# Optimization experiments

Measured on AMD Instinct MI355X. Metric: run time of the kernel, lower is better.

## Reference

```python
import jax, jax.numpy as jnp
import numpy as np

D_MODEL = 1024
NUM_HEADS = 16
D_K = D_MODEL // NUM_HEADS
SCALE = float(np.sqrt(D_K))


def setup_inputs() -> dict:
    key = jax.random.key(0)
    ks = jax.random.split(key, 11)
    B, S, D = 2, 2048, D_MODEL
    def lin(kw):
        # xavier-uniform-ish weight, zero bias (matches torch init style)
        lim = float(np.sqrt(6.0 / (D + D)))
        return jax.random.uniform(kw, (D, D), jnp.float32, -lim, lim)
    return {
        "q": jax.random.normal(ks[0], (B, S, D), jnp.float32),
        "k": jax.random.normal(ks[1], (B, S, D), jnp.float32),
        "v": jax.random.normal(ks[2], (B, S, D), jnp.float32),
        "Wq": lin(ks[3]), "bq": jnp.zeros((D,), jnp.float32),
        "Wk": lin(ks[4]), "bk": jnp.zeros((D,), jnp.float32),
        "Wv": lin(ks[5]), "bv": jnp.zeros((D,), jnp.float32),
        "Wo": lin(ks[6]), "bo": jnp.zeros((D,), jnp.float32),
    }


def _split_heads(x):
    B, S, _ = x.shape
    return x.reshape(B, S, NUM_HEADS, D_K).transpose(0, 2, 1, 3)  # (B,H,S,dk)


def reference(q, k, v, Wq, bq, Wk, bk, Wv, bv, Wo, bo):
    # torch nn.Linear: y = x @ W.T + b
    Q = _split_heads(q @ Wq.T + bq)
    K = _split_heads(k @ Wk.T + bk)
    V = _split_heads(v @ Wv.T + bv)
    scores = jnp.einsum("bhqd,bhkd->bhqk", Q, K) / SCALE
    # numerically-stable softmax with detached max (as in the torch code)
    m = jax.lax.stop_gradient(jnp.max(scores, axis=-1, keepdims=True))
    exp_scores = jnp.exp(scores - m)
    attn = exp_scores / (jnp.sum(exp_scores, axis=-1, keepdims=True) + 1e-9)
    out = jnp.einsum("bhqk,bhkd->bhqd", attn, V)  # (B,H,S,dk)
    B, H, S, dk = out.shape
    out = out.transpose(0, 2, 1, 3).reshape(B, S, H * dk)
    return out @ Wo.T + bo
```

## Files before the change

### kernel.cpp

```cpp
#include <hip/hip_runtime.h>


#define D_MODEL 1024
#define NHEADS  16
#define DKH     64
#define SEQ     2048
#define BATCH   2
#define MTOT    (BATCH * SEQ)
#define XE      ((long)MTOT * D_MODEL)
#define WE      ((long)D_MODEL * D_MODEL)
#define QSCALE  0.18033688011112042f

typedef __attribute__((ext_vector_type(8))) short short8v;
typedef __attribute__((ext_vector_type(4))) short short4v;
typedef __attribute__((ext_vector_type(4))) float f32x4;

typedef __attribute__((address_space(1))) void as1_void;
typedef __attribute__((address_space(3))) void as3_void;

__device__ __forceinline__ void gload16(const void* g, void* l) {
    __builtin_amdgcn_global_load_lds((const as1_void*)g, (as3_void*)l, 16, 0, 0);
}

__device__ __forceinline__ unsigned short f2bf(float x) {
    unsigned int u = __float_as_uint(x);
    u += 0x7FFFu + ((u >> 16) & 1u);
    return (unsigned short)(u >> 16);
}

__device__ __forceinline__ float fexp2(float x) {
    return __builtin_amdgcn_exp2f(x);
}

__device__ __forceinline__ unsigned int cvt_pk_bf16(float lo, float hi) {
    unsigned int r;
    asm("v_cvt_pk_bf16_f32 %0, %1, %2" : "=v"(r) : "v"(lo), "v"(hi));
    return r;
}

__device__ __forceinline__ int swz_u(int row, int col) {
    int byte = (col << 1) ^ ((row & 7) << 4);
    return (row << 6) + (byte >> 1);
}

__device__ __forceinline__ int swz_v(int d, int kv) {
    int slot = (d & 6) | ((d >> 3) & 1);
    int byte = (kv << 1) ^ (slot << 4);
    return (d << 6) + (byte >> 1);
}

struct ConvArgs {
    const float*    src[4];
    unsigned short* dst[4];
    int             n4[4];
};

__global__ __launch_bounds__(256) void convert_kernel(ConvArgs a) {
    int z = blockIdx.y;
    const float4*   s = (const float4*)a.src[z];
    unsigned short* d = a.dst[z];
    int n = a.n4[z];
    for (int i = blockIdx.x * blockDim.x + threadIdx.x; i < n;
         i += gridDim.x * blockDim.x) {
        float4 v = s[i];
        ushort4 o;
        o.x = f2bf(v.x); o.y = f2bf(v.y); o.z = f2bf(v.z); o.w = f2bf(v.w);
        *(ushort4*)(d + 4L * i) = o;
    }
}

__global__ __launch_bounds__(256) void proj_kernel(
    const float* __restrict__ xq, const float* __restrict__ xk,
    const float* __restrict__ xv, const unsigned short* __restrict__ wb,
    const float* __restrict__ bq, const float* __restrict__ bk,
    const float* __restrict__ bv, unsigned short* __restrict__ qkv) {
    __shared__ unsigned short As[3 * 128 * 32];
    __shared__ unsigned short Bs[3 * 128 * 32];

    const int t    = threadIdx.x;
    const int lane = t & 63;
    const int w    = t >> 6;
    const int wm   = w >> 1, wn = w & 1;
    const int l15  = lane & 15, g = lane >> 4;

    const int bid = blockIdx.x;
    const int xcd = bid & 7;
    const int k   = bid >> 3;
    const int ty  = (xcd << 2) | (k & 3);
    const int tx  = (k >> 2) & 7;
    const int z   = k >> 5;
    const float* bias = (z == 0) ? bq : (z == 1) ? bk : bv;
    const float scale = (z == 0) ? QSCALE : 1.0f;

    const float* Af = (z == 0) ? xq : (z == 1) ? xk : xv;
    const unsigned short* Bm = wb + (long)z * WE;
    unsigned short*       C  = qkv + (long)z * XE;
    const long m0 = (long)ty * 128;
    const long n0 = (long)tx * 128;
    const int  K  = D_MODEL;

    f32x4 acc[4][4] = {};

    const int idx0 = t, idx1 = t + 256;
    const int r0 = idx0 >> 2, c0 = (idx0 & 3) * 8;
    const int r1 = idx1 >> 2, c1 = (idx1 & 3) * 8;

    float4 a0_[2], a1_[2];

#define PLOAD_A(k0)                                                        \
    {                                                                      \
        const float* s0 = Af + (m0 + r0) * K + (k0) + c0;                  \
        const float* s1 = Af + (m0 + r1) * K + (k0) + c1;                  \
        a0_[0] = *(const float4*)(s0);                                     \
        a1_[0] = *(const float4*)(s0 + 4);                                 \
        a0_[1] = *(const float4*)(s1);                                     \
        a1_[1] = *(const float4*)(s1 + 4);                                 \
    }

#define PSTAGE_B(k0, buf)                                                  \
    gload16(Bm + (n0 + r0) * K + (k0) + c0, &Bs[(buf) * 4096 + idx0 * 8]); \
    gload16(Bm + (n0 + r1) * K + (k0) + c1, &Bs[(buf) * 4096 + idx1 * 8]);

#define PWRITE_A(buf)                                                      \
    {                                                                      \
        uint4 pk;                                                          \
        pk.x = cvt_pk_bf16(a0_[0].x, a0_[0].y);                            \
        pk.y = cvt_pk_bf16(a0_[0].z, a0_[0].w);                            \
        pk.z = cvt_pk_bf16(a1_[0].x, a1_[0].y);                            \
        pk.w = cvt_pk_bf16(a1_[0].z, a1_[0].w);                            \
        *(uint4*)&As[(buf) * 4096 + idx0 * 8] = pk;                        \
        pk.x = cvt_pk_bf16(a0_[1].x, a0_[1].y);                            \
        pk.y = cvt_pk_bf16(a0_[1].z, a0_[1].w);                            \
        pk.z = cvt_pk_bf16(a1_[1].x, a1_[1].y);                            \
        pk.w = cvt_pk_bf16(a1_[1].z, a1_[1].w);                            \
        *(uint4*)&As[(buf) * 4096 + idx1 * 8] = pk;                        \
    }

    PLOAD_A(0);
    PSTAGE_B(0, 0);
    PWRITE_A(0);
    int cur = 0;

    for (int it = 0; it < K / 32; ++it) {
        const int nxt = (cur == 2) ? 0 : cur + 1;
        const int kn  = ((it + 1) * 32) & (K - 1);
        PLOAD_A(kn);
        PSTAGE_B(kn, nxt);
        asm volatile("s_waitcnt vmcnt(6)" ::: "memory");
        asm volatile("s_waitcnt lgkmcnt(0)" ::: "memory");
        __builtin_amdgcn_sched_barrier(0);
        __builtin_amdgcn_s_barrier();
        __builtin_amdgcn_sched_barrier(0);

        const unsigned short* Ab = &As[cur * 4096];
        const unsigned short* Bb = &Bs[cur * 4096];

        short8v af[4], bf_[4];
#pragma unroll
        for (int mf = 0; mf < 4; ++mf)
            af[mf] = *(const short8v*)&Ab[(wm * 64 + mf * 16 + l15) * 32 + g * 8];
#pragma unroll
        for (int nf = 0; nf < 4; ++nf)
            bf_[nf] = *(const short8v*)&Bb[(wn * 64 + nf * 16 + l15) * 32 + g * 8];
        __builtin_amdgcn_s_setprio(1);
#pragma unroll
        for (int mf = 0; mf < 4; ++mf)
#pragma unroll
            for (int nf = 0; nf < 4; ++nf)
                acc[mf][nf] = __builtin_amdgcn_mfma_f32_16x16x32_bf16(
                    af[mf], bf_[nf], acc[mf][nf], 0, 0, 0);
        __builtin_amdgcn_s_setprio(0);

        PWRITE_A(nxt);
        cur = nxt;
    }

    float bvv[4];
#pragma unroll
    for (int nf = 0; nf < 4; ++nf)
        bvv[nf] = bias[n0 + wn * 64 + nf * 16 + l15];

#pragma unroll
    for (int mf = 0; mf < 4; ++mf)
#pragma unroll
        for (int nf = 0; nf < 4; ++nf)
#pragma unroll
            for (int r = 0; r < 4; ++r) {
                long row = m0 + wm * 64 + mf * 16 + g * 4 + r;
                long col = n0 + wn * 64 + nf * 16 + l15;
                C[row * (long)D_MODEL + col] =
                    f2bf((acc[mf][nf][r] + bvv[nf]) * scale);
            }
#undef PLOAD_A
#undef PSTAGE_B
#undef PWRITE_A
}

__global__ __launch_bounds__(256) void out_kernel(
    const unsigned short* __restrict__ ob, const unsigned short* __restrict__ wo,
    const float* __restrict__ bo, float* __restrict__ out) {
    __shared__ unsigned short As[3 * 128 * 32];
    __shared__ unsigned short Bs[3 * 128 * 32];

    const int t    = threadIdx.x;
    const int lane = t & 63;
    const int w    = t >> 6;
    const int wm   = w >> 1, wn = w & 1;
    const int l15  = lane & 15, g = lane >> 4;

    const int bid = blockIdx.x;
    const int xcd = bid & 7;
    const int k   = bid >> 3;
    const long m0 = (long)((xcd << 2) | (k & 3)) * 128;
    const long n0 = (long)(k >> 2) * 128;
    const int  K  = D_MODEL, N = D_MODEL;

    f32x4 acc[4][4] = {};

    const int idx0 = t, idx1 = t + 256;
    const int r0 = idx0 >> 2, c0 = (idx0 & 3) * 8;
    const int r1 = idx1 >> 2, c1 = (idx1 & 3) * 8;
    const unsigned short* pa0 = ob + (m0 + r0) * K + c0;
    const unsigned short* pa1 = ob + (m0 + r1) * K + c1;
    const unsigned short* pb0 = wo + (n0 + r0) * K + c0;
    const unsigned short* pb1 = wo + (n0 + r1) * K + c1;

#define OSTAGE(k0, buf)                                                    \
    gload16(pa0 + (k0), &As[(buf) * 4096 + idx0 * 8]);                     \
    gload16(pa1 + (k0), &As[(buf) * 4096 + idx1 * 8]);                     \
    gload16(pb0 + (k0), &Bs[(buf) * 4096 + idx0 * 8]);                     \
    gload16(pb1 + (k0), &Bs[(buf) * 4096 + idx1 * 8]);

    OSTAGE(0, 0);
    int cur = 0;

    for (int it = 0; it < K / 32; ++it) {
        const int nxt = (cur == 2) ? 0 : cur + 1;
        const int kn  = ((it + 1) * 32) & (K - 1);
        OSTAGE(kn, nxt);
        asm volatile("s_waitcnt vmcnt(4)" ::: "memory");
        __builtin_amdgcn_sched_barrier(0);
        __builtin_amdgcn_s_barrier();
        __builtin_amdgcn_sched_barrier(0);

        const unsigned short* Ab = &As[cur * 4096];
        const unsigned short* Bb = &Bs[cur * 4096];

        short8v af[4], bf_[4];
#pragma unroll
        for (int mf = 0; mf < 4; ++mf)
            af[mf] = *(const short8v*)&Ab[(wm * 64 + mf * 16 + l15) * 32 + g * 8];
#pragma unroll
        for (int nf = 0; nf < 4; ++nf)
            bf_[nf] = *(const short8v*)&Bb[(wn * 64 + nf * 16 + l15) * 32 + g * 8];
        __builtin_amdgcn_s_setprio(1);
#pragma unroll
        for (int mf = 0; mf < 4; ++mf)
#pragma unroll
            for (int nf = 0; nf < 4; ++nf)
                acc[mf][nf] = __builtin_amdgcn_mfma_f32_16x16x32_bf16(
                    af[mf], bf_[nf], acc[mf][nf], 0, 0, 0);
        __builtin_amdgcn_s_setprio(0);
        cur = nxt;
    }

    float bvv[4];
#pragma unroll
    for (int nf = 0; nf < 4; ++nf)
        bvv[nf] = bo[n0 + wn * 64 + nf * 16 + l15];

#pragma unroll
    for (int mf = 0; mf < 4; ++mf)
#pragma unroll
        for (int nf = 0; nf < 4; ++nf)
#pragma unroll
            for (int r = 0; r < 4; ++r) {
                long row = m0 + wm * 64 + mf * 16 + g * 4 + r;
                long col = n0 + wn * 64 + nf * 16 + l15;
                out[row * (long)N + col] = acc[mf][nf][r] + bvv[nf];
            }
#undef OSTAGE
}

#define KVB 4096

__global__ __launch_bounds__(512) void attn_kernel(
    const unsigned short* __restrict__ Qb, const unsigned short* __restrict__ Kb,
    const unsigned short* __restrict__ Vb, unsigned short* __restrict__ Ob) {
    __shared__ alignas(16) unsigned short Ks[2 * KVB];
    __shared__ alignas(16) unsigned short Vt[2 * KVB];
    __shared__ alignas(16) unsigned short Ps[8][16 * 64];
    __shared__ alignas(16) float corrS[8][16];

    const int t = threadIdx.x, lane = t & 63, w = t >> 6;
    const int l15 = lane & 15, g = lane >> 4;
    const int bid = blockIdx.x;
    const int xcd = bid & 7;
    const int kk2 = bid >> 3;
    const int bh  = (xcd << 2) | (kk2 & 3);
    const int qb  = kk2 >> 2;
    const long headoff = (long)(bh >> 4) * SEQ * D_MODEL + (long)(bh & 15) * DKH;
    const int q0w = qb * 128 + w * 16;

    short8v qf[2];
#pragma unroll
    for (int ks = 0; ks < 2; ++ks)
        qf[ks] = *(const short8v*)(Qb + headoff +
            (long)(q0w + l15) * D_MODEL + ks * 32 + g * 8);

    short8v onesv;
#pragma unroll
    for (int j = 0; j < 8; ++j) onesv[j] = (short)0x3F80;

    f32x4 o[4] = {};
    f32x4 ol = {};
    float mrun = -3.0e38f;

    const int vd0  = (t & 31) * 2;
    const int vkv0 = (t >> 5) * 4;
    const int kr0 = t >> 3, ks0 = t & 7;

    unsigned int va[4];

#define ISSUE_V(kt)                                                        \
    _Pragma("unroll")                                                      \
    for (int j = 0; j < 4; ++j)                                            \
        va[j] = *(const unsigned int*)(Vb + headoff +                      \
            (long)((kt) + vkv0 + j) * D_MODEL + vd0);

#define ISSUE_K(kt, off)                                                   \
    gload16(Kb + headoff + (long)((kt) + kr0) * D_MODEL +                  \
                ((ks0 ^ (kr0 & 7)) << 3), &Ks[(off) + t * 8]);

#define WRITE_V(off)                                                       \
    {                                                                      \
        short4v ra, rb;                                                    \
        _Pragma("unroll")                                                  \
        for (int j = 0; j < 4; ++j) {                                      \
            ra[j] = (short)(va[j] & 0xffffu);                              \
            rb[j] = (short)(va[j] >> 16);                                  \
        }                                                                  \
        *(short4v*)&Vt[(off) + swz_v(vd0,     vkv0)] = ra;                 \
        *(short4v*)&Vt[(off) + swz_v(vd0 + 1, vkv0)] = rb;                 \
    }

    asm volatile("s_waitcnt vmcnt(0)" ::: "memory");
    ISSUE_V(0);
    ISSUE_K(0, 0);
    WRITE_V(0);
    int cur = 0;

    for (int it = 0; it < SEQ / 64; ++it) {
        const int nxt = cur ^ 1;
        const int ktn = (((it + 1) & (SEQ / 64 - 1))) * 64;
        ISSUE_V(ktn);
        ISSUE_K(ktn, nxt * KVB);
        asm volatile("s_waitcnt vmcnt(5)" ::: "memory");
        asm volatile("s_waitcnt lgkmcnt(0)" ::: "memory");
        __builtin_amdgcn_sched_barrier(0);
        __builtin_amdgcn_s_barrier();
        __builtin_amdgcn_sched_barrier(0);

        const int kO = cur * KVB;

        f32x4 st[4] = {};
        __builtin_amdgcn_s_setprio(1);
#pragma unroll
        for (int ks = 0; ks < 2; ++ks)
#pragma unroll
            for (int mf = 0; mf < 4; ++mf) {
                short8v kf = *(const short8v*)&Ks[kO + swz_u(mf * 16 + l15, ks * 32 + g * 8)];
                st[mf] = __builtin_amdgcn_mfma_f32_16x16x32_bf16(
                    kf, qf[ks], st[mf], 0, 0, 0);
            }
        __builtin_amdgcn_s_setprio(0);

        float vmax = st[0][0];
#pragma unroll
        for (int mf = 0; mf < 4; ++mf)
#pragma unroll
            for (int r = 0; r < 4; ++r)
                vmax = fmaxf(vmax, st[mf][r]);
        vmax = fmaxf(vmax, __shfl_xor(vmax, 16));
        vmax = fmaxf(vmax, __shfl_xor(vmax, 32));

        const bool grow = __any(vmax > mrun + 8.0f);
        if (grow) {
            float mnew = fmaxf(mrun, vmax);
            float corr = fexp2(mrun - mnew);
            mrun = mnew;
            if (g == 0) corrS[w][l15] = corr;
        }

#pragma unroll
        for (int mf = 0; mf < 4; ++mf)
#pragma unroll
            for (int r = 0; r < 4; ++r)
                st[mf][r] = fexp2(st[mf][r] - mrun);

        unsigned short* Pw = Ps[w];
#pragma unroll
        for (int mf = 0; mf < 4; ++mf) {
            uint2 pk;
            pk.x = cvt_pk_bf16(st[mf][0], st[mf][1]);
            pk.y = cvt_pk_bf16(st[mf][2], st[mf][3]);
            *(uint2*)&Pw[swz_u(l15, mf * 16 + g * 4)] = pk;
        }

        if (grow) {
            float4 cv = *(const float4*)&corrS[w][g * 4];
#pragma unroll
            for (int nd = 0; nd < 4; ++nd)
#pragma unroll
                for (int r = 0; r < 4; ++r)
                    o[nd][r] *= cv[r];
#pragma unroll
            for (int r = 0; r < 4; ++r) ol[r] *= cv[r];
        }

        __builtin_amdgcn_s_setprio(1);
#pragma unroll
        for (int ks2 = 0; ks2 < 2; ++ks2) {
            short8v pf = *(const short8v*)&Pw[swz_u(l15, ks2 * 32 + g * 8)];
            ol = __builtin_amdgcn_mfma_f32_16x16x32_bf16(
                pf, onesv, ol, 0, 0, 0);
#pragma unroll
            for (int nd = 0; nd < 4; ++nd) {
                short8v vf = *(const short8v*)&Vt[kO + swz_v(nd * 16 + l15, ks2 * 32 + g * 8)];
                o[nd] = __builtin_amdgcn_mfma_f32_16x16x32_bf16(
                    pf, vf, o[nd], 0, 0, 0);
            }
        }
        __builtin_amdgcn_s_setprio(0);

        WRITE_V(nxt * KVB);
        cur = nxt;
    }

#pragma unroll
    for (int r = 0; r < 4; ++r) {
        float inv = 1.f / (ol[r] + 1e-9f);
        long rowoff = headoff + (long)(q0w + g * 4 + r) * D_MODEL;
#pragma unroll
        for (int nd = 0; nd < 4; ++nd)
            Ob[rowoff + nd * 16 + l15] = f2bf(o[nd][r] * inv);
    }
#undef ISSUE_V
#undef ISSUE_K
#undef WRITE_V
}

extern "C" void kernel_launch(void* const* d_in, const int* in_sizes, int n_in,
                              void* d_out, int out_size, void* d_ws, size_t ws_size,
                              hipStream_t stream) {
    unsigned short* ws  = (unsigned short*)d_ws;
    unsigned short* wb  = ws;
    unsigned short* qkv = ws + 4L * WE;
    unsigned short* ob  = qkv + 3L * XE;

    ConvArgs ca;
    ca.src[0] = (const float*)d_in[3]; ca.dst[0] = wb;           ca.n4[0] = (int)(WE / 4);
    ca.src[1] = (const float*)d_in[5]; ca.dst[1] = wb + WE;      ca.n4[1] = (int)(WE / 4);
    ca.src[2] = (const float*)d_in[7]; ca.dst[2] = wb + 2L * WE; ca.n4[2] = (int)(WE / 4);
    ca.src[3] = (const float*)d_in[9]; ca.dst[3] = wb + 3L * WE; ca.n4[3] = (int)(WE / 4);

    hipLaunchKernelGGL(convert_kernel, dim3(512, 4), dim3(256), 0, stream, ca);

    hipLaunchKernelGGL(proj_kernel, dim3(768), dim3(256), 0, stream,
                       (const float*)d_in[0], (const float*)d_in[1],
                       (const float*)d_in[2], wb,
                       (const float*)d_in[4], (const float*)d_in[6],
                       (const float*)d_in[8], qkv);

    hipLaunchKernelGGL(attn_kernel, dim3(512), dim3(512), 0, stream,
                       qkv, qkv + XE, qkv + 2L * XE, ob);

    hipLaunchKernelGGL(out_kernel, dim3(256), dim3(256), 0, stream,
                       ob, wb + 3L * WE, (const float*)d_in[10], (float*)d_out);
}
```

Measured before the change: 123.4 us.

## Deepen prefetch pipelines in QKV projection and output GEMM kernels

In the QKV projection GEMM, the loop is unrolled by two and alternates between two register sets for the fp32 A tile, so A is loaded two k-steps ahead while B is staged one step ahead. The wait count is relaxed to match. In the output projection GEMM, LDS buffering goes from three to four stages, with global-to-LDS loads issued two k-steps ahead. Both changes aim to hide more global-memory latency behind MFMA work, at the cost of more registers and LDS, which could reduce occupancy.

```diff
diff --git a/kernel.cpp b/kernel.cpp
--- a/kernel.cpp
+++ b/kernel.cpp
@@ -105,74 +105,93 @@
     const int r0 = idx0 >> 2, c0 = (idx0 & 3) * 8;
     const int r1 = idx1 >> 2, c1 = (idx1 & 3) * 8;
 
-    float4 a0_[2], a1_[2];
-
-#define PLOAD_A(k0)                                                        \
+    float4 ax0_[2], ax1_[2];
+    float4 ay0_[2], ay1_[2];
+
+#define PLOAD(S0, S1, k0)                                                  \
     {                                                                      \
         const float* s0 = Af + (m0 + r0) * K + (k0) + c0;                  \
         const float* s1 = Af + (m0 + r1) * K + (k0) + c1;                  \
-        a0_[0] = *(const float4*)(s0);                                     \
-        a1_[0] = *(const float4*)(s0 + 4);                                 \
-        a0_[1] = *(const float4*)(s1);                                     \
-        a1_[1] = *(const float4*)(s1 + 4);                                 \
+        S0[0] = *(const float4*)(s0);                                      \
+        S1[0] = *(const float4*)(s0 + 4);                                  \
+        S0[1] = *(const float4*)(s1);                                      \
+        S1[1] = *(const float4*)(s1 + 4);                                  \
     }
 
 #define PSTAGE_B(k0, buf)                                                  \
     gload16(Bm + (n0 + r0) * K + (k0) + c0, &Bs[(buf) * 4096 + idx0 * 8]); \
     gload16(Bm + (n0 + r1) * K + (k0) + c1, &Bs[(buf) * 4096 + idx1 * 8]);
 
-#define PWRITE_A(buf)                                                      \
+#define PWRITE(S0, S1, buf)                                                \
     {                                                                      \
         uint4 pk;                                                          \
-        pk.x = cvt_pk_bf16(a0_[0].x, a0_[0].y);                            \
-        pk.y = cvt_pk_bf16(a0_[0].z, a0_[0].w);                            \
-        pk.z = cvt_pk_bf16(a1_[0].x, a1_[0].y);                            \
-        pk.w = cvt_pk_bf16(a1_[0].z, a1_[0].w);                            \
+        pk.x = cvt_pk_bf16(S0[0].x, S0[0].y);                              \
+        pk.y = cvt_pk_bf16(S0[0].z, S0[0].w);                              \
+        pk.z = cvt_pk_bf16(S1[0].x, S1[0].y);                              \
+        pk.w = cvt_pk_bf16(S1[0].z, S1[0].w);                              \
         *(uint4*)&As[(buf) * 4096 + idx0 * 8] = pk;                        \
-        pk.x = cvt_pk_bf16(a0_[1].x, a0_[1].y);                            \
-        pk.y = cvt_pk_bf16(a0_[1].z, a0_[1].w);                            \
-        pk.z = cvt_pk_bf16(a1_[1].x, a1_[1].y);                            \
-        pk.w = cvt_pk_bf16(a1_[1].z, a1_[1].w);                            \
+        pk.x = cvt_pk_bf16(S0[1].x, S0[1].y);                              \
+        pk.y = cvt_pk_bf16(S0[1].z, S0[1].w);                              \
+        pk.z = cvt_pk_bf16(S1[1].x, S1[1].y);                              \
+        pk.w = cvt_pk_bf16(S1[1].z, S1[1].w);                              \
         *(uint4*)&As[(buf) * 4096 + idx1 * 8] = pk;                        \
     }
 
-    PLOAD_A(0);
+#define PCOMPUTE(buf)                                                      \
+    {                                                                      \
+        const unsigned short* Ab = &As[(buf) * 4096];                      \
+        const unsigned short* Bb = &Bs[(buf) * 4096];                      \
+        short8v af[4], bf_[4];                                             \
+        _Pragma("unroll")                                                  \
+        for (int mf = 0; mf < 4; ++mf)                                     \
+            af[mf] = *(const short8v*)&Ab[(wm * 64 + mf * 16 + l15) * 32 + g * 8]; \
+        _Pragma("unroll")                                                  \
+        for (int nf = 0; nf < 4; ++nf)                                     \
+            bf_[nf] = *(const short8v*)&Bb[(wn * 64 + nf * 16 + l15) * 32 + g * 8]; \
+        __builtin_amdgcn_s_setprio(1);                                     \
+        _Pragma("unroll")                                                  \
+        for (int mf = 0; mf < 4; ++mf)                                     \
+            _Pragma("unroll")                                              \
+            for (int nf = 0; nf < 4; ++nf)                                 \
+                acc[mf][nf] = __builtin_amdgcn_mfma_f32_16x16x32_bf16(     \
+                    af[mf], bf_[nf], acc[mf][nf], 0, 0, 0);                \
+        __builtin_amdgcn_s_setprio(0);                                     \
+    }
+
+#define PBAR()                                                             \
+    asm volatile("s_waitcnt vmcnt(10)" ::: "memory");                      \
+    asm volatile("s_waitcnt lgkmcnt(0)" ::: "memory");                     \
+    __builtin_amdgcn_sched_barrier(0);                                     \
+    __builtin_amdgcn_s_barrier();                                          \
+    __builtin_amdgcn_sched_barrier(0);
+
     PSTAGE_B(0, 0);
-    PWRITE_A(0);
+    PLOAD(ax0_, ax1_, 0);
+    PWRITE(ax0_, ax1_, 0);
+    PLOAD(ay0_, ay1_, 32);
     int cur = 0;
 
-    for (int it = 0; it < K / 32; ++it) {
-        const int nxt = (cur == 2) ? 0 : cur + 1;
-        const int kn  = ((it + 1) * 32) & (K - 1);
-        PLOAD_A(kn);
-        PSTAGE_B(kn, nxt);
-        asm volatile("s_waitcnt vmcnt(6)" ::: "memory");
-        asm volatile("s_waitcnt lgkmcnt(0)" ::: "memory");
-        __builtin_amdgcn_sched_barrier(0);
-        __builtin_amdgcn_s_barrier();
-        __builtin_amdgcn_sched_barrier(0);
-
-        const unsigned short* Ab = &As[cur * 4096];
-        const unsigned short* Bb = &Bs[cur * 4096];
-
-        short8v af[4], bf_[4];
-#pragma unroll
-        for (int mf = 0; mf < 4; ++mf)
-            af[mf] = *(const short8v*)&Ab[(wm * 64 + mf * 16 + l15) * 32 + g * 8];
-#pragma unroll
-        for (int nf = 0; nf < 4; ++nf)
-            bf_[nf] = *(const short8v*)&Bb[(wn * 64 + nf * 16 + l15) * 32 + g * 8];
-        __builtin_amdgcn_s_setprio(1);
-#pragma unroll
-        for (int mf = 0; mf < 4; ++mf)
-#pragma unroll
-            for (int nf = 0; nf < 4; ++nf)
-                acc[mf][nf] = __builtin_amdgcn_mfma_f32_16x16x32_bf16(
-                    af[mf], bf_[nf], acc[mf][nf], 0, 0, 0);
-        __builtin_amdgcn_s_setprio(0);
-
-        PWRITE_A(nxt);
-        cur = nxt;
+    for (int it = 0; it < K / 32; it += 2) {
+        {
+            const int nxt = (cur == 2) ? 0 : cur + 1;
+            PSTAGE_B(((it + 1) * 32) & (K - 1), nxt);
+            __builtin_amdgcn_sched_barrier(0);
+            PLOAD(ax0_, ax1_, ((it + 2) * 32) & (K - 1));
+            PBAR();
+            PCOMPUTE(cur);
+            PWRITE(ay0_, ay1_, nxt);
+            cur = nxt;
+        }
+        {
+            const int nxt = (cur == 2) ? 0 : cur + 1;
+            PSTAGE_B(((it + 2) * 32) & (K - 1), nxt);
+            __builtin_amdgcn_sched_barrier(0);
+            PLOAD(ay0_, ay1_, ((it + 3) * 32) & (K - 1));
+            PBAR();
+            PCOMPUTE(cur);
+            PWRITE(ax0_, ax1_, nxt);
+            cur = nxt;
+        }
     }
 
     float bvv[4];
@@ -191,16 +210,18 @@
                 C[row * (long)D_MODEL + col] =
                     f2bf((acc[mf][nf][r] + bvv[nf]) * scale);
             }
-#undef PLOAD_A
+#undef PLOAD
 #undef PSTAGE_B
-#undef PWRITE_A
+#undef PWRITE
+#undef PCOMPUTE
+#undef PBAR
 }
 
 __global__ __launch_bounds__(256) void out_kernel(
     const unsigned short* __restrict__ ob, const unsigned short* __restrict__ wo,
     const float* __restrict__ bo, float* __restrict__ out) {
-    __shared__ unsigned short As[3 * 128 * 32];
-    __shared__ unsigned short Bs[3 * 128 * 32];
+    __shared__ unsigned short As[4 * 128 * 32];
+    __shared__ unsigned short Bs[4 * 128 * 32];
 
     const int t    = threadIdx.x;
     const int lane = t & 63;
@@ -232,13 +253,14 @@
     gload16(pb1 + (k0), &Bs[(buf) * 4096 + idx1 * 8]);
 
     OSTAGE(0, 0);
+    OSTAGE(32, 1);
     int cur = 0;
 
     for (int it = 0; it < K / 32; ++it) {
-        const int nxt = (cur == 2) ? 0 : cur + 1;
-        const int kn  = ((it + 1) * 32) & (K - 1);
-        OSTAGE(kn, nxt);
-        asm volatile("s_waitcnt vmcnt(4)" ::: "memory");
+        const int nn = (cur + 2) & 3;
+        const int kn = ((it + 2) * 32) & (K - 1);
+        OSTAGE(kn, nn);
+        asm volatile("s_waitcnt vmcnt(8)" ::: "memory");
         __builtin_amdgcn_sched_barrier(0);
         __builtin_amdgcn_s_barrier();
         __builtin_amdgcn_sched_barrier(0);
@@ -261,7 +283,7 @@
                 acc[mf][nf] = __builtin_amdgcn_mfma_f32_16x16x32_bf16(
                     af[mf], bf_[nf], acc[mf][nf], 0, 0, 0);
         __builtin_amdgcn_s_setprio(0);
-        cur = nxt;
+        cur = (cur + 1) & 3;
     }
 
     float bvv[4];
```

New measurement: 122.5 us. Within noise of the previous version (-0.7%).
